# Optimization experiments

Measured on AMD Instinct MI355X. Metric: run time of the kernel, lower is better.

## Reference

```python
import jax, jax.numpy as jnp
import numpy as np

B, V, C, H, W = 4, 4, 20, 240, 320
M, N = 500000, 2000000   # unique voxels, full points
P, D, K = 100000, 64, 1024  # points per batch, proj dim, num_matches
TAU = 0.07
NEG = -1.0e6


def setup_inputs() -> dict:
    key = jax.random.key(0)
    ks = jax.random.split(key, 12)
    cam_3d_F = jax.random.normal(ks[0], (M, C), jnp.float32)
    cam_2d = jax.random.normal(ks[1], (B * V, C, H, W), jnp.float32)
    feat_proj_3d = jax.random.normal(ks[2], (B, P, D), jnp.float32)
    feat_detach_2d = jax.random.normal(ks[3], (B, P, D), jnp.float32)
    feat_proj_2d = jax.random.normal(ks[4], (B, P, D), jnp.float32)
    feat_detach_3d = jax.random.normal(ks[5], (B, P, D), jnp.float32)
    labels_cls_3d = (jax.random.uniform(ks[6], (B, C)) < 0.7).astype(jnp.float32).at[:, 0].set(1.0)
    labels_cls_2d = (jax.random.uniform(ks[7], (B, C)) < 0.7).astype(jnp.float32).at[:, 0].set(1.0)
    inverse_map = jax.random.randint(ks[8], (N,), 0, M)
    batch_idx = jnp.sort(jax.random.randint(ks[9], (N,), 0, B))
    # sample-without-replacement indices (np.random.choice replace=False analogue)
    match_idx_3d = jax.vmap(lambda k: jax.random.permutation(k, P)[:K])(jax.random.split(ks[10], B))
    match_idx_2d = jax.vmap(lambda k: jax.random.permutation(k, P)[:K])(jax.random.split(ks[11], B))
    return {
        "cam_3d_F": cam_3d_F, "cam_2d": cam_2d,
        "feat_proj_3d": feat_proj_3d, "feat_detach_2d": feat_detach_2d,
        "feat_proj_2d": feat_proj_2d, "feat_detach_3d": feat_detach_3d,
        "labels_cls_3d": labels_cls_3d, "labels_cls_2d": labels_cls_2d,
        "inverse_map": inverse_map, "batch_idx": batch_idx,
        "match_idx_3d": match_idx_3d, "match_idx_2d": match_idx_2d,
    }


def _soft_margin(x, y):
    # F.multilabel_soft_margin_loss: mean over classes then batch == overall mean
    return -jnp.mean(y * jax.nn.log_sigmoid(x) + (1.0 - y) * jax.nn.log_sigmoid(-x))


def _cmg_loss(fea_k, fea_q, idx):
    # fea_*: [B,P,D], idx: [B,K] -> InfoNCE with identity targets, summed over batches
    k = jnp.take_along_axis(fea_k, idx[:, :, None], axis=1)  # [B,K,D]
    q = jnp.take_along_axis(fea_q, idx[:, :, None], axis=1)  # [B,K,D]
    def one(kb, qb):
        logits = jnp.einsum('kd,md->km', kb, qb) / TAU  # [K,K]
        return -jnp.mean(jnp.diagonal(jax.nn.log_softmax(logits, axis=1)))
    return jnp.sum(jax.vmap(one)(k, q))


def reference(cam_3d_F, cam_2d, feat_proj_3d, feat_detach_2d, feat_proj_2d,
              feat_detach_3d, labels_cls_3d, labels_cls_2d,
              inverse_map, batch_idx, match_idx_3d, match_idx_2d):
    # ---- multi_class_loss_3d: gather + per-batch segment mean ----
    cam_full = cam_3d_F[inverse_map]                                   # [N,C]
    seg_sum = jax.ops.segment_sum(cam_full, batch_idx, num_segments=B)  # [B,C]
    cnt = jax.ops.segment_sum(jnp.ones((cam_full.shape[0],), cam_full.dtype),
                              batch_idx, num_segments=B)                # [B]
    cls_feat = seg_sum / cnt[:, None]
    loss_cam_3d = _soft_margin(cls_feat, labels_cls_3d)
    lab_full = labels_cls_3d[batch_idx]                                # [N,C]
    result_3d = jax.nn.softmax(cam_full + (1.0 - lab_full) * NEG, axis=1)
    # ---- multi_class_loss_2d ----
    cam2 = cam_2d.reshape(B, V, C, H, W).transpose(0, 2, 3, 4, 1)      # [B,C,H,W,V]
    predict_2d = cam2.mean(axis=(2, 3, 4))                             # mean over V then HxW
    loss_cam_2d = _soft_margin(predict_2d, labels_cls_2d)
    lab2 = labels_cls_2d[:, :, None, None, None]                       # [B,C,1,1,1]
    result_2d = jax.nn.softmax(cam2 + (1.0 - lab2) * NEG, axis=1)
    # ---- CMG contrastive losses (q side detached in the original) ----
    loss_cmg_3d = _cmg_loss(feat_proj_3d, jax.lax.stop_gradient(feat_detach_2d), match_idx_3d)
    loss_cmg_2d = _cmg_loss(feat_proj_2d, jax.lax.stop_gradient(feat_detach_3d), match_idx_2d)
    # warm weights and loss weights all 1.0 (post-warmup)
    loss = loss_cam_3d + loss_cam_2d + loss_cmg_3d + loss_cmg_2d
    return (loss, result_3d, result_2d)
```

## Files before the change

kernel.cpp:

```cpp
#include <hip/hip_runtime.h>

#define FLT_NEG_MAX -3.402823466e38f
#define NEGC -1000000.0f
#define INV_TAU (1.0f/0.07f)

static const long long NN = 2000000LL;

#define WS_KBUF 256
#define WS_PM   (WS_KBUF + 524288)
#define WS_PS   (WS_PM + 131072)
#define WS_DIAG (WS_PS + 131072)

__device__ __forceinline__ float wave_sum64(float v) {
  v += __shfl_xor(v, 1, 64);
  v += __shfl_xor(v, 2, 64);
  v += __shfl_xor(v, 4, 64);
  v += __shfl_xor(v, 8, 64);
  v += __shfl_xor(v, 16, 64);
  v += __shfl_xor(v, 32, 64);
  return v;
}
__device__ __forceinline__ float wave_max64(float v) {
  v = fmaxf(v, __shfl_xor(v, 1, 64));
  v = fmaxf(v, __shfl_xor(v, 2, 64));
  v = fmaxf(v, __shfl_xor(v, 4, 64));
  v = fmaxf(v, __shfl_xor(v, 8, 64));
  v = fmaxf(v, __shfl_xor(v, 16, 64));
  v = fmaxf(v, __shfl_xor(v, 32, 64));
  return v;
}
__device__ __forceinline__ float logsig(float x) {
  float z = -x;
  return -(fmaxf(z, 0.0f) + log1pf(__expf(-fabsf(z))));
}

__global__ __launch_bounds__(256) void kA(const float* __restrict__ cam3d,
                                          const float* __restrict__ lab3_g,
                                          const int* __restrict__ inv_map,
                                          const int* __restrict__ bidx,
                                          float* __restrict__ out_r3,
                                          float* __restrict__ acc) {
  __shared__ float lab3[80];
  __shared__ float bins[84];
  __shared__ float stage[4][64 * 21];
  const int tid = threadIdx.x;
  if (tid < 80) lab3[tid] = lab3_g[tid];
  if (tid < 84) bins[tid] = 0.0f;
  __syncthreads();
  const int wid = tid >> 6, lane = tid & 63;

  float racc[20];
  #pragma unroll
  for (int c = 0; c < 20; ++c) racc[c] = 0.0f;
  float rcnt = 0.0f;
  int rb_cur = -1;

  const long long stride = (long long)gridDim.x * 256LL;
  for (long long base = (long long)blockIdx.x * 256LL; base < NN; base += stride) {
    long long n = base + tid;
    bool active = (n < NN);
    float x[20];
    int b = 0;
    if (active) {
      int iv = inv_map[n];
      b = bidx[n];
      const float4* rp = reinterpret_cast<const float4*>(cam3d + (long long)iv * 20LL);
      #pragma unroll
      for (int q = 0; q < 5; ++q) {
        float4 t4 = rp[q];
        x[4*q+0] = t4.x; x[4*q+1] = t4.y; x[4*q+2] = t4.z; x[4*q+3] = t4.w;
      }
    } else {
      #pragma unroll
      for (int c = 0; c < 20; ++c) x[c] = 0.0f;
    }
    int b0 = __shfl(b, 0, 64);
    bool uni = __all(active) && __all(b == b0);
    if (uni) {
      if (b0 != rb_cur) {
        if (rb_cur >= 0) {
          #pragma unroll
          for (int c = 0; c < 20; ++c) {
            float v = wave_sum64(racc[c]);
            if (lane == 0) atomicAdd(&bins[rb_cur * 20 + c], v);
            racc[c] = 0.0f;
          }
          if (lane == 0) atomicAdd(&bins[80 + rb_cur], rcnt * 64.0f);
          rcnt = 0.0f;
        }
        rb_cur = b0;
      }
      #pragma unroll
      for (int c = 0; c < 20; ++c) racc[c] += x[c];
      rcnt += 1.0f;
    } else if (active) {
      #pragma unroll
      for (int c = 0; c < 20; ++c) atomicAdd(&bins[b * 20 + c], x[c]);
      atomicAdd(&bins[80 + b], 1.0f);
    }
    if (active) {
      float mx = FLT_NEG_MAX;
      #pragma unroll
      for (int c = 0; c < 20; ++c) {
        x[c] += (1.0f - lab3[b * 20 + c]) * NEGC;
        mx = fmaxf(mx, x[c]);
      }
      float s = 0.0f;
      #pragma unroll
      for (int c = 0; c < 20; ++c) { x[c] = __expf(x[c] - mx); s += x[c]; }
      float is = 1.0f / s;
      #pragma unroll
      for (int c = 0; c < 20; ++c) x[c] *= is;
    }
    __syncthreads();
    #pragma unroll
    for (int c = 0; c < 20; ++c) stage[wid][lane * 21 + c] = x[c];
    __syncthreads();
    long long nw = base + (long long)wid * 64LL;
    long long rem = NN - nw;
    int valid = rem >= 64 ? 64 : (rem > 0 ? (int)rem : 0);
    if (valid > 0) {
      int lim = valid * 20;
      #pragma unroll
      for (int j = 0; j < 20; ++j) {
        int idx = lane + 64 * j;
        if (idx < lim) {
          int rl = idx / 20;
          int cc = idx - rl * 20;
          __builtin_nontemporal_store(stage[wid][rl * 21 + cc],
                                      &out_r3[nw * 20LL + idx]);
        }
      }
    }
  }
  if (rb_cur >= 0) {
    #pragma unroll
    for (int c = 0; c < 20; ++c) {
      float v = wave_sum64(racc[c]);
      if (lane == 0) atomicAdd(&bins[rb_cur * 20 + c], v);
    }
    if (lane == 0) atomicAdd(&bins[80 + rb_cur], rcnt * 64.0f);
  }
  __syncthreads();
  if (tid < 84) atomicAdd(&acc[tid], bins[tid]);
}

__global__ __launch_bounds__(256) void kB(const float* __restrict__ cam2d,
                                          const float* __restrict__ lab2_g,
                                          float* __restrict__ out_r2,
                                          float* __restrict__ acc) {
  const int bid = blockIdx.x;
  const int b = bid / 1200;
  const int rem = bid - b * 1200;
  const int h = rem / 5;
  const int wt = rem - h * 5;
  const int t = threadIdx.x;
  const int wid = t >> 6;
  const int lane = t & 63;
  const int w = wt * 64 + lane;
  __shared__ float bins2[20];
  __shared__ float trans[20][320];
  if (t < 20) bins2[t] = 0.0f;
  __syncthreads();
  const float* inb = cam2d + ((long long)(b * 4 + wid) * 20LL) * 76800LL
                   + (long long)h * 320 + w;
  float x[20];
  #pragma unroll
  for (int c = 0; c < 20; ++c) x[c] = inb[(long long)c * 76800LL];
  #pragma unroll
  for (int c = 0; c < 20; ++c) {
    float s = wave_sum64(x[c]);
    if (lane == 0) atomicAdd(&bins2[c], s);
  }
  float mx = FLT_NEG_MAX;
  #pragma unroll
  for (int c = 0; c < 20; ++c) {
    x[c] += (1.0f - lab2_g[b * 20 + c]) * NEGC;
    mx = fmaxf(mx, x[c]);
  }
  float s = 0.0f;
  #pragma unroll
  for (int c = 0; c < 20; ++c) { x[c] = __expf(x[c] - mx); s += x[c]; }
  float is = 1.0f / s;
  #pragma unroll
  for (int c = 0; c < 20; ++c) trans[c][lane * 5 + wid] = x[c] * is;
  __syncthreads();
  const long long obase = (long long)b * 6144000LL + ((long long)h * 320 + wt * 64) * 4LL;
  #pragma unroll
  for (int c = 0; c < 20; ++c)
    __builtin_nontemporal_store(trans[c][(t >> 2) * 5 + (t & 3)],
                                &out_r2[obase + (long long)c * 307200LL + t]);
  if (t < 20) atomicAdd(&acc[84 + b * 20 + t], bins2[t]);
}

__global__ __launch_bounds__(256) void kC(const float* __restrict__ fp3,
                                          const float* __restrict__ fp2,
                                          const int* __restrict__ mi3,
                                          const int* __restrict__ mi2,
                                          float* __restrict__ kbuf) {
  int g = blockIdx.x * 256 + threadIdx.x;
  int row = g >> 4;
  int d4 = g & 15;
  int pair = row >> 10;
  int l = pair >> 2, b = pair & 3;
  int i = row & 1023;
  int idx = l ? mi2[b * 1024 + i] : mi3[b * 1024 + i];
  const float* src = l ? fp2 : fp3;
  const float4* s4 = reinterpret_cast<const float4*>(src + ((long long)b * 100000 + idx) * 64LL);
  reinterpret_cast<float4*>(kbuf)[(long long)row * 16 + d4] = s4[d4];
}

__global__ __launch_bounds__(256) void kD(const float* __restrict__ kbuf,
                                          const float* __restrict__ fd2,
                                          const float* __restrict__ fd3,
                                          const int* __restrict__ mi3,
                                          const int* __restrict__ mi2,
                                          float* __restrict__ pm,
                                          float* __restrict__ ps,
                                          float* __restrict__ diag) {
  const int wglob = blockIdx.x * 4 + (threadIdx.x >> 6);
  const int lane = threadIdx.x & 63;
  const int pair = wglob >> 9;
  const int cb = (wglob >> 5) & 15;
  const int rb = wglob & 31;
  const int l = pair >> 2, b = pair & 3;
  const int colg = cb * 64 + lane;
  const int qi = l ? mi2[b * 1024 + colg] : mi3[b * 1024 + colg];
  const float* fq = l ? fd3 : fd2;
  const float4* q4 = reinterpret_cast<const float4*>(fq + ((long long)b * 100000 + qi) * 64LL);
  float4 q[16];
  #pragma unroll
  for (int d = 0; d < 16; ++d) q[d] = q4[d];
  const float* kbase = kbuf + ((long long)pair * 1024 + rb * 32) * 64LL;
  float m_keep = 0.0f, s_keep = 0.0f;
  for (int r = 0; r < 32; ++r) {
    const float4* kr = reinterpret_cast<const float4*>(kbase + r * 64);
    float a0 = 0, a1 = 0, a2 = 0, a3 = 0;
    #pragma unroll
    for (int d = 0; d < 16; ++d) {
      float4 kv = kr[d];
      a0 = fmaf(kv.x, q[d].x, a0);
      a1 = fmaf(kv.y, q[d].y, a1);
      a2 = fmaf(kv.z, q[d].z, a2);
      a3 = fmaf(kv.w, q[d].w, a3);
    }
    float vlog = (a0 + a1 + a2 + a3) * INV_TAU;
    int rowg = rb * 32 + r;
    if (colg == rowg) diag[pair * 1024 + rowg] = vlog;
    float mx = wave_max64(vlog);
    float se = wave_sum64(__expf(vlog - mx));
    if (lane == r) { m_keep = mx; s_keep = se; }
  }
  if (lane < 32) {
    int off = (pair * 16 + cb) * 1024 + rb * 32 + lane;
    pm[off] = m_keep;
    ps[off] = s_keep;
  }
}

__global__ __launch_bounds__(256) void kE(const float* __restrict__ pm,
                                          const float* __restrict__ ps,
                                          const float* __restrict__ diag,
                                          float* __restrict__ acc) {
  const int row = blockIdx.x * 256 + threadIdx.x;
  const int pair = row >> 10;
  const int rl = row & 1023;
  const int l = pair >> 2;
  float m = FLT_NEG_MAX, s = 0.0f;
  #pragma unroll
  for (int cb = 0; cb < 16; ++cb) {
    float mm = pm[(pair * 16 + cb) * 1024 + rl];
    float ss = ps[(pair * 16 + cb) * 1024 + rl];
    if (mm > m) { s = s * __expf(m - mm) + ss; m = mm; }
    else        { s += ss * __expf(mm - m); }
  }
  float r = diag[row] - (m + __logf(s));
  float t = wave_sum64(r);
  __shared__ float wsum[4];
  if ((threadIdx.x & 63) == 0) wsum[threadIdx.x >> 6] = t;
  __syncthreads();
  if (threadIdx.x == 0)
    atomicAdd(&acc[164 + l], wsum[0] + wsum[1] + wsum[2] + wsum[3]);
}

__global__ __launch_bounds__(256) void kF(const float* __restrict__ acc,
                                          const float* __restrict__ lab3,
                                          const float* __restrict__ lab2,
                                          float* __restrict__ out_loss) {
  const int t = threadIdx.x;
  float term = 0.0f;
  if (t < 80) {
    int b = t / 20;
    float x = acc[t] / acc[80 + b];
    float y = lab3[t];
    term = y * logsig(x) + (1.0f - y) * logsig(-x);
  } else if (t < 160) {
    int i = t - 80;
    float x = acc[84 + i] * (1.0f / 307200.0f);
    float y = lab2[i];
    term = y * logsig(x) + (1.0f - y) * logsig(-x);
  }
  float tsum = wave_sum64(term);
  __shared__ float wsum[4];
  if ((t & 63) == 0) wsum[t >> 6] = tsum;
  __syncthreads();
  if (t == 0) {
    float total = wsum[0] + wsum[1] + wsum[2] + wsum[3];
    float margin = -total / 80.0f;
    float cmg = -(acc[164] + acc[165]) / 1024.0f;
    out_loss[0] = margin + cmg;
  }
}

extern "C" void kernel_launch(void* const* d_in, const int* in_sizes, int n_in,
                              void* d_out, int out_size, void* d_ws, size_t ws_size,
                              hipStream_t stream) {
  (void)in_sizes; (void)n_in; (void)out_size; (void)ws_size;
  const float* cam3d = (const float*)d_in[0];
  const float* cam2d = (const float*)d_in[1];
  const float* fp3   = (const float*)d_in[2];
  const float* fd2   = (const float*)d_in[3];
  const float* fp2   = (const float*)d_in[4];
  const float* fd3   = (const float*)d_in[5];
  const float* lab3  = (const float*)d_in[6];
  const float* lab2  = (const float*)d_in[7];
  const int* invm    = (const int*)d_in[8];
  const int* bidx    = (const int*)d_in[9];
  const int* mi3     = (const int*)d_in[10];
  const int* mi2     = (const int*)d_in[11];

  float* out      = (float*)d_out;
  float* out_loss = out;
  float* out_r3   = out + 1;
  float* out_r2   = out + 1 + 40000000LL;

  float* acc  = (float*)d_ws;
  float* kbuf = acc + WS_KBUF;
  float* pm   = acc + WS_PM;
  float* psb  = acc + WS_PS;
  float* diag = acc + WS_DIAG;

  hipMemsetAsync(d_ws, 0, 1024, stream);

  kA<<<1792, 256, 0, stream>>>(cam3d, lab3, invm, bidx, out_r3, acc);
  kB<<<4800, 256, 0, stream>>>(cam2d, lab2, out_r2, acc);
  kC<<<512, 256, 0, stream>>>(fp3, fp2, mi3, mi2, kbuf);
  kD<<<1024, 256, 0, stream>>>(kbuf, fd2, fd3, mi3, mi2, pm, psb, diag);
  kE<<<32, 256, 0, stream>>>(pm, psb, diag, acc);
  kF<<<1, 256, 0, stream>>>(acc, lab3, lab2, out_loss);
}
```

Measured before the change: 716.7 us.

## Fuse 3D CAM, 2D CAM and feature gather into one launch

Merges the three independent first-stage kernels into one grid, with block-index ranges dispatching to the 3D softmax/segment-sum work, the 2D softmax work and the match-feature gather. This removes two launch boundaries and lets the short gather and 2D blocks overlap with the tail of the 3D work. The 2D path is also remapped so each thread handles one (w, view) pair and writes the transposed output directly, with no shared-memory transpose. The cost is that input reads become 64-byte segments spread across four views instead of full 256-byte rows. All blocks now reserve the largest shared-memory footprint, which may limit occupancy.

```diff
diff --git a/kernel.cpp b/kernel.cpp
--- a/kernel.cpp
+++ b/kernel.cpp
@@ -10,6 +10,10 @@
 #define WS_PM   (WS_KBUF + 524288)
 #define WS_PS   (WS_PM + 131072)
 #define WS_DIAG (WS_PS + 131072)
+
+#define NB_A 1792
+#define NB_B 4800
+#define NB_C 512
 
 __device__ __forceinline__ float wave_sum64(float v) {
   v += __shfl_xor(v, 1, 64);
@@ -34,180 +38,178 @@
   return -(fmaxf(z, 0.0f) + log1pf(__expf(-fabsf(z))));
 }
 
-__global__ __launch_bounds__(256) void kA(const float* __restrict__ cam3d,
-                                          const float* __restrict__ lab3_g,
-                                          const int* __restrict__ inv_map,
-                                          const int* __restrict__ bidx,
-                                          float* __restrict__ out_r3,
-                                          float* __restrict__ acc) {
-  __shared__ float lab3[80];
-  __shared__ float bins[84];
-  __shared__ float stage[4][64 * 21];
+__global__ __launch_bounds__(256) void mega1(const float* __restrict__ cam3d,
+                                             const float* __restrict__ lab3_g,
+                                             const int* __restrict__ inv_map,
+                                             const int* __restrict__ bidx,
+                                             float* __restrict__ out_r3,
+                                             const float* __restrict__ cam2d,
+                                             const float* __restrict__ lab2_g,
+                                             float* __restrict__ out_r2,
+                                             const float* __restrict__ fp3,
+                                             const float* __restrict__ fp2,
+                                             const int* __restrict__ mi3,
+                                             const int* __restrict__ mi2,
+                                             float* __restrict__ kbuf,
+                                             float* __restrict__ acc) {
+  __shared__ float smem[5540];
   const int tid = threadIdx.x;
-  if (tid < 80) lab3[tid] = lab3_g[tid];
-  if (tid < 84) bins[tid] = 0.0f;
-  __syncthreads();
+  const int bid = blockIdx.x;
   const int wid = tid >> 6, lane = tid & 63;
 
-  float racc[20];
-  #pragma unroll
-  for (int c = 0; c < 20; ++c) racc[c] = 0.0f;
-  float rcnt = 0.0f;
-  int rb_cur = -1;
-
-  const long long stride = (long long)gridDim.x * 256LL;
-  for (long long base = (long long)blockIdx.x * 256LL; base < NN; base += stride) {
-    long long n = base + tid;
-    bool active = (n < NN);
-    float x[20];
-    int b = 0;
-    if (active) {
-      int iv = inv_map[n];
-      b = bidx[n];
-      const float4* rp = reinterpret_cast<const float4*>(cam3d + (long long)iv * 20LL);
+  if (bid < NB_A) {
+    float* lab3 = smem;
+    float* bins = smem + 80;
+    float* stage = smem + 164;
+    if (tid < 80) lab3[tid] = lab3_g[tid];
+    if (tid < 84) bins[tid] = 0.0f;
+    __syncthreads();
+
+    float racc[20];
+    #pragma unroll
+    for (int c = 0; c < 20; ++c) racc[c] = 0.0f;
+    float rcnt = 0.0f;
+    int rb_cur = -1;
+
+    const long long stride = (long long)NB_A * 256LL;
+    for (long long base = (long long)bid * 256LL; base < NN; base += stride) {
+      long long n = base + tid;
+      bool active = (n < NN);
+      float x[20];
+      int b = 0;
+      if (active) {
+        int iv = inv_map[n];
+        b = bidx[n];
+        const float4* rp = reinterpret_cast<const float4*>(cam3d + (long long)iv * 20LL);
+        #pragma unroll
+        for (int q = 0; q < 5; ++q) {
+          float4 t4 = rp[q];
+          x[4*q+0] = t4.x; x[4*q+1] = t4.y; x[4*q+2] = t4.z; x[4*q+3] = t4.w;
+        }
+      } else {
+        #pragma unroll
+        for (int c = 0; c < 20; ++c) x[c] = 0.0f;
+      }
+      int b0 = __shfl(b, 0, 64);
+      bool uni = __all(active) && __all(b == b0);
+      if (uni) {
+        if (b0 != rb_cur) {
+          if (rb_cur >= 0) {
+            #pragma unroll
+            for (int c = 0; c < 20; ++c) {
+              float v = wave_sum64(racc[c]);
+              if (lane == 0) atomicAdd(&bins[rb_cur * 20 + c], v);
+              racc[c] = 0.0f;
+            }
+            if (lane == 0) atomicAdd(&bins[80 + rb_cur], rcnt * 64.0f);
+            rcnt = 0.0f;
+          }
+          rb_cur = b0;
+        }
+        #pragma unroll
+        for (int c = 0; c < 20; ++c) racc[c] += x[c];
+        rcnt += 1.0f;
+      } else if (active) {
+        #pragma unroll
+        for (int c = 0; c < 20; ++c) atomicAdd(&bins[b * 20 + c], x[c]);
+        atomicAdd(&bins[80 + b], 1.0f);
+      }
+      if (active) {
+        float mx = FLT_NEG_MAX;
+        #pragma unroll
+        for (int c = 0; c < 20; ++c) {
+          x[c] += (1.0f - lab3[b * 20 + c]) * NEGC;
+          mx = fmaxf(mx, x[c]);
+        }
+        float s = 0.0f;
+        #pragma unroll
+        for (int c = 0; c < 20; ++c) { x[c] = __expf(x[c] - mx); s += x[c]; }
+        float is = 1.0f / s;
+        #pragma unroll
+        for (int c = 0; c < 20; ++c) x[c] *= is;
+      }
+      __syncthreads();
       #pragma unroll
-      for (int q = 0; q < 5; ++q) {
-        float4 t4 = rp[q];
-        x[4*q+0] = t4.x; x[4*q+1] = t4.y; x[4*q+2] = t4.z; x[4*q+3] = t4.w;
-      }
-    } else {
-      #pragma unroll
-      for (int c = 0; c < 20; ++c) x[c] = 0.0f;
-    }
-    int b0 = __shfl(b, 0, 64);
-    bool uni = __all(active) && __all(b == b0);
-    if (uni) {
-      if (b0 != rb_cur) {
-        if (rb_cur >= 0) {
-          #pragma unroll
-          for (int c = 0; c < 20; ++c) {
-            float v = wave_sum64(racc[c]);
-            if (lane == 0) atomicAdd(&bins[rb_cur * 20 + c], v);
-            racc[c] = 0.0f;
+      for (int c = 0; c < 20; ++c) stage[wid * 1344 + lane * 21 + c] = x[c];
+      __syncthreads();
+      long long nw = base + (long long)wid * 64LL;
+      long long rem = NN - nw;
+      int valid = rem >= 64 ? 64 : (rem > 0 ? (int)rem : 0);
+      if (valid > 0) {
+        int lim = valid * 20;
+        #pragma unroll
+        for (int j = 0; j < 20; ++j) {
+          int idx = lane + 64 * j;
+          if (idx < lim) {
+            int rl = idx / 20;
+            int cc = idx - rl * 20;
+            __builtin_nontemporal_store(stage[wid * 1344 + rl * 21 + cc],
+                                        &out_r3[nw * 20LL + idx]);
           }
-          if (lane == 0) atomicAdd(&bins[80 + rb_cur], rcnt * 64.0f);
-          rcnt = 0.0f;
         }
-        rb_cur = b0;
-      }
-      #pragma unroll
-      for (int c = 0; c < 20; ++c) racc[c] += x[c];
-      rcnt += 1.0f;
-    } else if (active) {
-      #pragma unroll
-      for (int c = 0; c < 20; ++c) atomicAdd(&bins[b * 20 + c], x[c]);
-      atomicAdd(&bins[80 + b], 1.0f);
-    }
-    if (active) {
-      float mx = FLT_NEG_MAX;
+      }
+    }
+    if (rb_cur >= 0) {
       #pragma unroll
       for (int c = 0; c < 20; ++c) {
-        x[c] += (1.0f - lab3[b * 20 + c]) * NEGC;
-        mx = fmaxf(mx, x[c]);
-      }
-      float s = 0.0f;
-      #pragma unroll
-      for (int c = 0; c < 20; ++c) { x[c] = __expf(x[c] - mx); s += x[c]; }
-      float is = 1.0f / s;
-      #pragma unroll
-      for (int c = 0; c < 20; ++c) x[c] *= is;
+        float v = wave_sum64(racc[c]);
+        if (lane == 0) atomicAdd(&bins[rb_cur * 20 + c], v);
+      }
+      if (lane == 0) atomicAdd(&bins[80 + rb_cur], rcnt * 64.0f);
     }
     __syncthreads();
-    #pragma unroll
-    for (int c = 0; c < 20; ++c) stage[wid][lane * 21 + c] = x[c];
+    if (tid < 84) atomicAdd(&acc[tid], bins[tid]);
+
+  } else if (bid < NB_A + NB_B) {
+    const int rb = bid - NB_A;
+    const int b = rb / 1200;
+    const int rem = rb - b * 1200;
+    const int h = rem / 5;
+    const int wt = rem - h * 5;
+    const int wl = tid >> 2, v = tid & 3;
+    const int w = wt * 64 + wl;
+    float* bins2 = smem;
+    if (tid < 20) bins2[tid] = 0.0f;
     __syncthreads();
-    long long nw = base + (long long)wid * 64LL;
-    long long rem = NN - nw;
-    int valid = rem >= 64 ? 64 : (rem > 0 ? (int)rem : 0);
-    if (valid > 0) {
-      int lim = valid * 20;
-      #pragma unroll
-      for (int j = 0; j < 20; ++j) {
-        int idx = lane + 64 * j;
-        if (idx < lim) {
-          int rl = idx / 20;
-          int cc = idx - rl * 20;
-          __builtin_nontemporal_store(stage[wid][rl * 21 + cc],
-                                      &out_r3[nw * 20LL + idx]);
-        }
-      }
-    }
-  }
-  if (rb_cur >= 0) {
+    const float* inb = cam2d + ((long long)(b * 4 + v) * 20LL) * 76800LL
+                     + (long long)h * 320 + w;
+    float x[20];
+    #pragma unroll
+    for (int c = 0; c < 20; ++c) x[c] = inb[(long long)c * 76800LL];
     #pragma unroll
     for (int c = 0; c < 20; ++c) {
-      float v = wave_sum64(racc[c]);
-      if (lane == 0) atomicAdd(&bins[rb_cur * 20 + c], v);
-    }
-    if (lane == 0) atomicAdd(&bins[80 + rb_cur], rcnt * 64.0f);
-  }
-  __syncthreads();
-  if (tid < 84) atomicAdd(&acc[tid], bins[tid]);
-}
-
-__global__ __launch_bounds__(256) void kB(const float* __restrict__ cam2d,
-                                          const float* __restrict__ lab2_g,
-                                          float* __restrict__ out_r2,
-                                          float* __restrict__ acc) {
-  const int bid = blockIdx.x;
-  const int b = bid / 1200;
-  const int rem = bid - b * 1200;
-  const int h = rem / 5;
-  const int wt = rem - h * 5;
-  const int t = threadIdx.x;
-  const int wid = t >> 6;
-  const int lane = t & 63;
-  const int w = wt * 64 + lane;
-  __shared__ float bins2[20];
-  __shared__ float trans[20][320];
-  if (t < 20) bins2[t] = 0.0f;
-  __syncthreads();
-  const float* inb = cam2d + ((long long)(b * 4 + wid) * 20LL) * 76800LL
-                   + (long long)h * 320 + w;
-  float x[20];
-  #pragma unroll
-  for (int c = 0; c < 20; ++c) x[c] = inb[(long long)c * 76800LL];
-  #pragma unroll
-  for (int c = 0; c < 20; ++c) {
-    float s = wave_sum64(x[c]);
-    if (lane == 0) atomicAdd(&bins2[c], s);
-  }
-  float mx = FLT_NEG_MAX;
-  #pragma unroll
-  for (int c = 0; c < 20; ++c) {
-    x[c] += (1.0f - lab2_g[b * 20 + c]) * NEGC;
-    mx = fmaxf(mx, x[c]);
-  }
-  float s = 0.0f;
-  #pragma unroll
-  for (int c = 0; c < 20; ++c) { x[c] = __expf(x[c] - mx); s += x[c]; }
-  float is = 1.0f / s;
-  #pragma unroll
-  for (int c = 0; c < 20; ++c) trans[c][lane * 5 + wid] = x[c] * is;
-  __syncthreads();
-  const long long obase = (long long)b * 6144000LL + ((long long)h * 320 + wt * 64) * 4LL;
-  #pragma unroll
-  for (int c = 0; c < 20; ++c)
-    __builtin_nontemporal_store(trans[c][(t >> 2) * 5 + (t & 3)],
-                                &out_r2[obase + (long long)c * 307200LL + t]);
-  if (t < 20) atomicAdd(&acc[84 + b * 20 + t], bins2[t]);
-}
-
-__global__ __launch_bounds__(256) void kC(const float* __restrict__ fp3,
-                                          const float* __restrict__ fp2,
-                                          const int* __restrict__ mi3,
-                                          const int* __restrict__ mi2,
-                                          float* __restrict__ kbuf) {
-  int g = blockIdx.x * 256 + threadIdx.x;
-  int row = g >> 4;
-  int d4 = g & 15;
-  int pair = row >> 10;
-  int l = pair >> 2, b = pair & 3;
-  int i = row & 1023;
-  int idx = l ? mi2[b * 1024 + i] : mi3[b * 1024 + i];
-  const float* src = l ? fp2 : fp3;
-  const float4* s4 = reinterpret_cast<const float4*>(src + ((long long)b * 100000 + idx) * 64LL);
-  reinterpret_cast<float4*>(kbuf)[(long long)row * 16 + d4] = s4[d4];
+      float s = wave_sum64(x[c]);
+      if (lane == 0) atomicAdd(&bins2[c], s);
+    }
+    float mx = FLT_NEG_MAX;
+    #pragma unroll
+    for (int c = 0; c < 20; ++c) {
+      x[c] += (1.0f - lab2_g[b * 20 + c]) * NEGC;
+      mx = fmaxf(mx, x[c]);
+    }
+    float s = 0.0f;
+    #pragma unroll
+    for (int c = 0; c < 20; ++c) { x[c] = __expf(x[c] - mx); s += x[c]; }
+    float is = 1.0f / s;
+    #pragma unroll
+    for (int c = 0; c < 20; ++c)
+      __builtin_nontemporal_store(x[c] * is,
+          &out_r2[(((long long)(b * 20 + c) * 240 + h) * 320 + w) * 4 + v]);
+    __syncthreads();
+    if (tid < 20) atomicAdd(&acc[84 + b * 20 + tid], bins2[tid]);
+
+  } else {
+    int g = (bid - NB_A - NB_B) * 256 + tid;
+    int row = g >> 4;
+    int d4 = g & 15;
+    int pair = row >> 10;
+    int l = pair >> 2, b = pair & 3;
+    int i = row & 1023;
+    int idx = l ? mi2[b * 1024 + i] : mi3[b * 1024 + i];
+    const float* src = l ? fp2 : fp3;
+    const float4* s4 = reinterpret_cast<const float4*>(src + ((long long)b * 100000 + idx) * 64LL);
+    reinterpret_cast<float4*>(kbuf)[(long long)row * 16 + d4] = s4[d4];
+  }
 }
 
 __global__ __launch_bounds__(256) void kD(const float* __restrict__ kbuf,
@@ -342,9 +344,9 @@
 
   hipMemsetAsync(d_ws, 0, 1024, stream);
 
-  kA<<<1792, 256, 0, stream>>>(cam3d, lab3, invm, bidx, out_r3, acc);
-  kB<<<4800, 256, 0, stream>>>(cam2d, lab2, out_r2, acc);
-  kC<<<512, 256, 0, stream>>>(fp3, fp2, mi3, mi2, kbuf);
+  mega1<<<NB_A + NB_B + NB_C, 256, 0, stream>>>(cam3d, lab3, invm, bidx, out_r3,
+                                                cam2d, lab2, out_r2,
+                                                fp3, fp2, mi3, mi2, kbuf, acc);
   kD<<<1024, 256, 0, stream>>>(kbuf, fd2, fd3, mi3, mi2, pm, psb, diag);
   kE<<<32, 256, 0, stream>>>(pm, psb, diag, acc);
   kF<<<1, 256, 0, stream>>>(acc, lab3, lab2, out_loss);
```

Measured after the change: 689.6 us. -3.8%, faster.
